# Performance work log

Hardware: AMD Instinct MI355X
Metric: run time of the kernel (lower is better)

Reference implementation:

```python
import jax, jax.numpy as jnp
import numpy as np

B, M, RPI = 16, 80, 256            # images, objects/image, relations/image
N, R = B * M, B * RPI
DF, REP, EMB, HID, NH, L = 12544, 1024, 256, 512, 8, 4
OBJC, RELC = 151, 51
IMW, IMH = 800.0, 600.0


def _ln(x, g, b):
    m = x.mean(-1, keepdims=True)
    v = ((x - m) ** 2).mean(-1, keepdims=True)
    return (x - m) * jax.lax.rsqrt(v + 1e-5) * g + b


def _encoder(x, qkv_w, qkv_b, out_w, out_b, f1_w, f1_b, f2_w, f2_b, ln1_s, ln1_b, ln2_s, ln2_b):
    # post-LN transformer encoder, L layers, x: [B, M, HID]
    Bb, Mm, D = x.shape
    dk = D // NH
    scale = 1.0 / jnp.sqrt(jnp.float32(dk))
    for l in range(L):
        qkv = x @ qkv_w[l].T + qkv_b[l]
        q, k, v = jnp.split(qkv, 3, axis=-1)
        hs = lambda t: t.reshape(Bb, Mm, NH, dk).transpose(0, 2, 1, 3)
        q, k, v = hs(q), hs(k), hs(v)
        att = jax.nn.softmax(jnp.einsum('bhqd,bhkd->bhqk', q, k) * scale, axis=-1)
        o = jnp.einsum('bhqk,bhkd->bhqd', att, v).transpose(0, 2, 1, 3).reshape(Bb, Mm, D)
        x = _ln(x + o @ out_w[l].T + out_b[l], ln1_s[l], ln1_b[l])
        f = jax.nn.relu(x @ f1_w[l].T + f1_b[l]) @ f2_w[l].T + f2_b[l]
        x = _ln(x + f, ln2_s[l], ln2_b[l])
    return x


def _box_info(boxes):
    wh = boxes[:, 2:] - boxes[:, :2] + 1.0
    xy = boxes[:, :2] + 0.5 * wh
    w, h = wh[:, :1], wh[:, 1:]
    x, y = xy[:, :1], xy[:, 1:]
    x1, y1, x2, y2 = boxes[:, 0:1], boxes[:, 1:2], boxes[:, 2:3], boxes[:, 3:4]
    return jnp.concatenate([w / IMW, h / IMH, x / IMW, y / IMH, x1 / IMW, y1 / IMH,
                            x2 / IMW, y2 / IMH, w * h / (IMW * IMH)], axis=-1)  # [N, 9]


def setup_inputs() -> dict:
    key = jax.random.key(0)
    ks = iter(jax.random.split(key, 80))
    nrm = lambda shape, s=0.02: jax.random.normal(next(ks), shape, jnp.float32) * s
    d = {}
    d['features'] = jax.random.normal(next(ks), (N, DF), jnp.float32)
    d['union_features'] = jax.random.normal(next(ks), (R, REP), jnp.float32)
    x1 = jax.random.uniform(next(ks), (N, 1)) * (IMW - 120.0)
    y1 = jax.random.uniform(next(ks), (N, 1)) * (IMH - 120.0)
    w = jax.random.uniform(next(ks), (N, 1)) * 100.0 + 5.0
    h = jax.random.uniform(next(ks), (N, 1)) * 100.0 + 5.0
    d['boxes'] = jnp.concatenate([x1, y1, x1 + w, y1 + h], axis=-1)
    d['logits'] = jax.random.normal(next(ks), (N, OBJC), jnp.float32)
    d['labels'] = jax.random.randint(next(ks), (N,), 0, OBJC)
    d['rel_pair_idxs'] = jax.random.randint(next(ks), (B, RPI, 2), 0, M)
    # feature extractor
    d['fe1_w'] = nrm((REP, DF)); d['fe1_b'] = jnp.zeros((REP,))
    d['fe2_w'] = nrm((REP, REP)); d['fe2_b'] = jnp.zeros((REP,))
    # embeddings
    d['emb1'] = nrm((OBJC, EMB), 1.0)
    d['emb2'] = nrm((OBJC, EMB), 1.0)
    # bbox embed 9->32->128
    d['bb1_w'] = nrm((32, 9)); d['bb1_b'] = jnp.zeros((32,))
    d['bb2_w'] = nrm((128, 32)); d['bb2_b'] = jnp.zeros((128,))
    d['lobj_w'] = nrm((HID, REP + EMB + 128)); d['lobj_b'] = jnp.zeros((HID,))
    d['ledge_w'] = nrm((HID, EMB + HID)); d['ledge_b'] = jnp.zeros((HID,))
    for p in ('o', 'e'):
        d[p + 'qkv_w'] = nrm((L, 3 * HID, HID)); d[p + 'qkv_b'] = jnp.zeros((L, 3 * HID))
        d[p + 'out_w'] = nrm((L, HID, HID)); d[p + 'out_b'] = jnp.zeros((L, HID))
        d[p + 'f1_w'] = nrm((L, HID, HID)); d[p + 'f1_b'] = jnp.zeros((L, HID))
        d[p + 'f2_w'] = nrm((L, HID, HID)); d[p + 'f2_b'] = jnp.zeros((L, HID))
        d[p + 'ln1_s'] = jnp.ones((L, HID)); d[p + 'ln1_b'] = jnp.zeros((L, HID))
        d[p + 'ln2_s'] = jnp.ones((L, HID)); d[p + 'ln2_b'] = jnp.zeros((L, HID))
    d['pcat_w'] = nrm((REP, 2 * HID)); d['pcat_b'] = jnp.zeros((REP,))
    d['fuse_w'] = nrm((REP, REP + HID)); d['fuse_b'] = jnp.zeros((REP,))
    d['cpx_w'] = nrm((RELC, 2 * REP)); d['cpx_b'] = jnp.zeros((RELC,))
    d['dpath_w'] = nrm((RELC, REP)); d['dpath_b'] = jnp.zeros((RELC,))
    return d


def reference(features, union_features, boxes, logits,
              fe1_w, fe1_b, fe2_w, fe2_b, emb1, emb2,
              bb1_w, bb1_b, bb2_w, bb2_b, lobj_w, lobj_b, ledge_w, ledge_b,
              oqkv_w, oqkv_b, oout_w, oout_b, of1_w, of1_b, of2_w, of2_b,
              oln1_s, oln1_b, oln2_s, oln2_b,
              eqkv_w, eqkv_b, eout_w, eout_b, ef1_w, ef1_b, ef2_w, ef2_b,
              eln1_s, eln1_b, eln2_s, eln2_b,
              pcat_w, pcat_b, fuse_w, fuse_b, cpx_w, cpx_b, dpath_w, dpath_b,
              labels, rel_pair_idxs):
    # FeatureExtractor
    bf = jax.nn.relu(features @ fe1_w.T + fe1_b)
    bf = jax.nn.relu(bf @ fe2_w.T + fe2_b)                        # [N, REP]
    # bbox embedding (dropout = identity in eval)
    pos = jax.nn.relu(_box_info(boxes) @ bb1_w.T + bb1_b)
    pos = jax.nn.relu(pos @ bb2_w.T + bb2_b)                      # [N, 128]
    obj_rep = jnp.concatenate([bf, emb1[labels], pos], -1) @ lobj_w.T + lobj_b  # [N, HID]
    obj_emb = _encoder(obj_rep.reshape(B, M, HID), oqkv_w, oqkv_b, oout_w, oout_b,
                       of1_w, of1_b, of2_w, of2_b, oln1_s, oln1_b, oln2_s, oln2_b)  # [B, M, HID]
    edge_in = jnp.concatenate([obj_emb.reshape(N, HID), emb2[labels]], -1) @ ledge_w.T + ledge_b
    gctx = _encoder(edge_in.reshape(B, M, HID), eqkv_w, eqkv_b, eout_w, eout_b,
                    ef1_w, ef1_b, ef2_w, ef2_b, eln1_s, eln1_b, eln2_s, eln2_b).mean(axis=1)  # [B, HID]
    # pair gather per image
    head = jax.vmap(lambda e, i: e[i])(obj_emb, rel_pair_idxs[:, :, 0])  # [B, RPI, HID]
    tail = jax.vmap(lambda e, i: e[i])(obj_emb, rel_pair_idxs[:, :, 1])
    pair = jnp.concatenate([head, tail], -1).reshape(R, 2 * HID)
    local = pair @ pcat_w.T + pcat_b                               # [R, REP]
    gexp = jnp.repeat(gctx, RPI, axis=0)                           # [R, HID]
    sem = jax.nn.relu(jnp.concatenate([local, gexp], -1) @ fuse_w.T + fuse_b)
    final = jnp.concatenate([sem, union_features], -1)             # [R, 2*REP]
    rel_logits = final @ cpx_w.T + cpx_b + local @ dpath_w.T + dpath_b  # [R, RELC]
    return rel_logits
```

## Files before the change

### kernel.cpp

```cpp
#include <hip/hip_runtime.h>
#include <hip/hip_bf16.h>
#include <cstdint>

#define DEV_INLINE __device__ __forceinline__

using u16 = unsigned short;
typedef __attribute__((ext_vector_type(8))) short bf8_t;
typedef __attribute__((ext_vector_type(4))) float f32x4;

constexpr int cB = 16, cM = 80, cRPI = 256;
constexpr int cN = cB * cM;
constexpr int cR = cB * cRPI;
constexpr int cDF = 12544, cREP = 1024, cEMB = 256, cHID = 512, cNH = 8, cL = 4;
constexpr int cRELC = 51;

DEV_INLINE u16 f2bf(float x) { return __builtin_bit_cast(u16, __float2bfloat16(x)); }
DEV_INLINE float bf2f(u16 u) { return __bfloat162float(__builtin_bit_cast(__hip_bfloat16, u)); }

DEV_INLINE float wave_max(float v) {
#pragma unroll
  for (int o = 32; o; o >>= 1) v = fmaxf(v, __shfl_xor(v, o));
  return v;
}
DEV_INLINE float wave_sum(float v) {
#pragma unroll
  for (int o = 32; o; o >>= 1) v += __shfl_xor(v, o);
  return v;
}

DEV_INLINE void gl_lds16(const u16* gp, char* lp) {
  __builtin_amdgcn_global_load_lds(
      (const __attribute__((address_space(1))) void*)gp,
      (__attribute__((address_space(3))) void*)lp, 16, 0, 0);
}

DEV_INLINE void xcd_remap(int& bx, int& by) {
  const int gx = gridDim.x;
  const int nwg = gx * gridDim.y;
  const int id = blockIdx.x + gx * blockIdx.y;
  const int q = nwg >> 3, r = nwg & 7;
  const int x = id & 7, k = id >> 3;
  const int idp = (x < r) ? x * (q + 1) + k : r * (q + 1) + (x - r) * q + k;
  bx = idp % gx;
  by = idp / gx;
}

__global__ __launch_bounds__(256) void gemm_aw(
    const u16* __restrict__ A,
    const u16* __restrict__ W, int ldw,
    float* __restrict__ outF, int ldc,
    u16* __restrict__ outH, int ldh,
    const float* __restrict__ bias,
    const float* __restrict__ res, int resld, int resmode,
    int relu)
{
  __shared__ u16 As[32 * 512];
  const int tid = threadIdx.x;
  const int wid = tid >> 6, lane = tid & 63;
  const int l15 = lane & 15, l4 = lane >> 4;
  int bx, by;
  xcd_remap(bx, by);
  const int bm = by * 32, bn = bx * 32;
  const int wr = wid >> 1, wc = wid & 1;

#pragma unroll
  for (int i = 0; i < 8; ++i) {
    const int c = i * 256 + tid;
    const int row = c >> 6, gran = c & 63;
    const int sg = gran ^ (row & 7);
    gl_lds16(A + (size_t)(bm + row) * 512 + sg * 8,
             (char*)As + (size_t)(i * 256 + wid * 64) * 16);
  }

  const u16* wrow = W + (size_t)(bn + wc * 16 + l15) * ldw + l4 * 8;
  bf8_t wv[16];
#pragma unroll
  for (int ks = 0; ks < 16; ++ks)
    wv[ks] = *(const bf8_t*)&wrow[ks * 32];

  __syncthreads();

  const int ra = wr * 16 + l15;
  f32x4 acc = {};
#pragma unroll
  for (int ks = 0; ks < 16; ++ks) {
    const int ga = ((ks << 2) | l4) ^ (ra & 7);
    const bf8_t af = *(const bf8_t*)&As[ra * 512 + ga * 8];
    acc = __builtin_amdgcn_mfma_f32_16x16x32_bf16(af, wv[ks], acc, 0, 0, 0);
  }

  const int ccol = bn + wc * 16 + l15;
  const float bv = bias ? bias[ccol] : 0.f;
#pragma unroll
  for (int g = 0; g < 4; ++g) {
    const int r = bm + wr * 16 + l4 * 4 + g;
    float v = acc[g] + bv;
    if (resmode == 1) v += res[(size_t)r * resld + ccol];
    if (relu) v = fmaxf(v, 0.f);
    if (outF) outF[(size_t)r * ldc + ccol] = v;
    if (outH) outH[(size_t)r * ldh + ccol] = f2bf(v);
  }
}

static void gaw(hipStream_t s, const u16* A, const u16* W, int ldw, int M, int N,
                float* outF, int ldc, u16* outH, int ldh,
                const float* bias, const float* res, int resld, int resmode, int relu) {
  dim3 g(N / 32, M / 32);
  gemm_aw<<<g, 256, 0, s>>>(A, W, ldw, outF, ldc, outH, ldh, bias, res, resld, resmode, relu);
}

template <int BM, int BN, bool SPLIT>
__global__ __launch_bounds__(256) void gemm_h(
    const u16* __restrict__ A, int lda,
    const u16* __restrict__ Bw, int ldb,
    int Mr, int Nr, int Klen,
    float* __restrict__ outF, int ldc,
    u16* __restrict__ outH, int ldh,
    const float* __restrict__ bias,
    const float* __restrict__ res, int resld, int resmode,
    int relu)
{
  constexpr int MF = BM > 32 ? BM / 32 : 1, NF = BN > 32 ? BN / 32 : 1;
  constexpr int ACH = BM * 4, BCH = BN * 4;
  __shared__ u16 As[2][BM * 32];
  __shared__ u16 Bs[2][BN * 32];
  const int tid = threadIdx.x;
  const int wid = tid >> 6, lane = tid & 63;
  const int l15 = lane & 15, l4 = lane >> 4;
  int bx, by;
  xcd_remap(bx, by);
  const int bm = by * BM, bn = bx * BN;
  const int wr = wid >> 1, wc = wid & 1;
  const int kbase = SPLIT ? blockIdx.z * Klen : 0;

  f32x4 acc[MF][NF] = {};

  auto stage = [&](int buf, int ks) {
    const int k0 = kbase + (ks << 5);
#pragma unroll
    for (int i = 0; i < (ACH + 255) / 256; ++i) {
      const int cA = i * 256 + tid;
      if (ACH % 256 == 0 || cA < ACH) {
        const int row = cA >> 2, seg = cA & 3;
        const int sseg = seg ^ (row & 3);
        gl_lds16(A + (size_t)(bm + row) * lda + k0 + sseg * 8,
                 (char*)As[buf] + (size_t)(cA - lane) * 16);
      }
    }
#pragma unroll
    for (int i = 0; i < (BCH + 255) / 256; ++i) {
      const int cBp = i * 256 + ((tid + 128) & 255);
      if (BCH % 256 == 0 || cBp < BCH) {
        const int row = cBp >> 2, seg = cBp & 3;
        const int sseg = seg ^ (row & 3);
        int brow = bn + row; if (brow > Nr - 1) brow = Nr - 1;
        gl_lds16(Bw + (size_t)brow * ldb + k0 + sseg * 8,
                 (char*)Bs[buf] + (size_t)(cBp - lane) * 16);
      }
    }
  };

  const int nk = Klen >> 5;
  stage(0, 0);
  __syncthreads();

  for (int ks = 0; ks < nk; ++ks) {
    const int cur = ks & 1;
    if (ks + 1 < nk) stage(cur ^ 1, ks + 1);

    bf8_t af[MF], bfr[NF];
#pragma unroll
    for (int m = 0; m < MF; ++m) {
      const int r = wr * (BM / 2) + m * 16 + l15;
      const int g = l4 ^ (r & 3);
      af[m] = *(const bf8_t*)&As[cur][r * 32 + g * 8];
    }
#pragma unroll
    for (int n = 0; n < NF; ++n) {
      const int r = wc * (BN / 2) + n * 16 + l15;
      const int g = l4 ^ (r & 3);
      bfr[n] = *(const bf8_t*)&Bs[cur][r * 32 + g * 8];
    }
#pragma unroll
    for (int m = 0; m < MF; ++m)
#pragma unroll
      for (int n = 0; n < NF; ++n)
        acc[m][n] = __builtin_amdgcn_mfma_f32_16x16x32_bf16(af[m], bfr[n], acc[m][n], 0, 0, 0);
    __syncthreads();
  }

  if (SPLIT) {
    float* po = outF + (size_t)blockIdx.z * Mr * ldc;
#pragma unroll
    for (int m = 0; m < MF; ++m)
#pragma unroll
      for (int n = 0; n < NF; ++n) {
        const int ccol = bn + wc * (BN / 2) + n * 16 + l15;
        if (ccol >= Nr) continue;
#pragma unroll
        for (int g = 0; g < 4; ++g) {
          const int r = bm + wr * (BM / 2) + m * 16 + l4 * 4 + g;
          po[(size_t)r * ldc + ccol] = acc[m][n][g];
        }
      }
  } else {
#pragma unroll
    for (int m = 0; m < MF; ++m)
#pragma unroll
      for (int n = 0; n < NF; ++n) {
        const int ccol = bn + wc * (BN / 2) + n * 16 + l15;
        if (ccol >= Nr) continue;
        const float bv = bias ? bias[ccol] : 0.f;
#pragma unroll
        for (int g = 0; g < 4; ++g) {
          const int r = bm + wr * (BM / 2) + m * 16 + l4 * 4 + g;
          float v = acc[m][n][g] + bv;
          if (resmode == 1) v += res[(size_t)r * resld + ccol];
          else if (resmode == 2) v += res[(size_t)(r >> 8) * resld + ccol];
          if (relu) v = fmaxf(v, 0.f);
          if (outF) outF[(size_t)r * ldc + ccol] = v;
          if (outH) outH[(size_t)r * ldh + ccol] = f2bf(v);
        }
      }
  }
}

template <int BM, int BN>
static void g16(hipStream_t s, const u16* A, int lda, const u16* W, int ldb,
                int M, int N, int K, float* outF, int ldc, u16* outH, int ldh,
                const float* bias, const float* res, int resld, int resmode, int relu) {
  dim3 g((N + BN - 1) / BN, M / BM);
  gemm_h<BM, BN, false><<<g, 256, 0, s>>>(A, lda, W, ldb, M, N, K, outF, ldc, outH, ldh,
                                          bias, res, resld, resmode, relu);
}

__global__ void conv_big2(const float* __restrict__ f, const float* __restrict__ w,
                          u16* __restrict__ fh, u16* __restrict__ wh) {
  constexpr int N1 = cN * cDF / 4;
  constexpr int N2 = cREP * cDF / 4;
  for (int i = blockIdx.x * 256 + threadIdx.x; i < N1 + N2; i += gridDim.x * 256) {
    const float4 v = (i < N1) ? ((const float4*)f)[i] : ((const float4*)w)[i - N1];
    ushort4 o = {f2bf(v.x), f2bf(v.y), f2bf(v.z), f2bf(v.w)};
    if (i < N1) ((ushort4*)fh)[i] = o; else ((ushort4*)wh)[i - N1] = o;
  }
}

constexpr size_t W_FE2 = 0, W_LOBJ = W_FE2 + 1048576, W_LEDGE = W_LOBJ + 720896,
  W_OQKV = W_LEDGE + 393216, W_OOUT = W_OQKV + 3145728, W_OF1 = W_OOUT + 1048576,
  W_OF2 = W_OF1 + 1048576, W_EQKV = W_OF2 + 1048576, W_EOUT = W_EQKV + 3145728,
  W_EF1 = W_EOUT + 1048576, W_EF2 = W_EF1 + 1048576, W_PCAT = W_EF2 + 1048576,
  W_FUSE = W_PCAT + 1048576, W_WEND = W_FUSE + 1572864;

struct EncSrcs {
  const float *fe2, *lobj, *ledge, *oqkv, *oout, *of1, *of2,
              *eqkv, *eout, *ef1, *ef2, *pcat, *fuse;
};

__global__ void conv_enc(EncSrcs S, u16* __restrict__ wb) {
#define SEG(nm, OFF, PRE, LEN) \
  if (i < (PRE) + (LEN)) { \
    const float4 v = ((const float4*)S.nm)[i - (PRE)]; \
    ushort4 o = {f2bf(v.x), f2bf(v.y), f2bf(v.z), f2bf(v.w)}; \
    ((ushort4*)(wb + (OFF)))[i - (PRE)] = o; \
  } else
  for (int i = blockIdx.x * 256 + threadIdx.x; i < (int)(W_WEND / 4); i += gridDim.x * 256) {
    SEG(fe2,  W_FE2,   0,       262144)
    SEG(lobj, W_LOBJ,  262144,  180224)
    SEG(ledge,W_LEDGE, 442368,  98304)
    SEG(oqkv, W_OQKV,  540672,  786432)
    SEG(oout, W_OOUT,  1327104, 262144)
    SEG(of1,  W_OF1,   1589248, 262144)
    SEG(of2,  W_OF2,   1851392, 262144)
    SEG(eqkv, W_EQKV,  2113536, 786432)
    SEG(eout, W_EOUT,  2899968, 262144)
    SEG(ef1,  W_EF1,   3162112, 262144)
    SEG(ef2,  W_EF2,   3424256, 262144)
    SEG(pcat, W_PCAT,  3686400, 262144)
    SEG(fuse, W_FUSE,  3948544, 393216)
    { }
  }
#undef SEG
}

__global__ void conv_cat(const float* __restrict__ cpx, const float* __restrict__ dpath,
                         const float* __restrict__ cb, const float* __restrict__ db,
                         u16* __restrict__ catw, float* __restrict__ biasc) {
  constexpr int N1 = cRELC * 512;
  constexpr int N2 = cRELC * 256;
  const int i0 = blockIdx.x * 256 + threadIdx.x;
  if (blockIdx.x == 0 && threadIdx.x < cRELC) biasc[threadIdx.x] = cb[threadIdx.x] + db[threadIdx.x];
  for (int i = i0; i < N1 + N2; i += gridDim.x * 256) {
    if (i < N1) {
      const int r = i >> 9, c = i & 511;
      const float4 v = ((const float4*)cpx)[i];
      ushort4 o = {f2bf(v.x), f2bf(v.y), f2bf(v.z), f2bf(v.w)};
      ((ushort4*)catw)[r * 768 + c] = o;
    } else {
      const int j = i - N1, r = j >> 8, c = j & 255;
      const float4 v = ((const float4*)dpath)[j];
      ushort4 o = {f2bf(v.x), f2bf(v.y), f2bf(v.z), f2bf(v.w)};
      ((ushort4*)catw)[r * 768 + 512 + c] = o;
    }
  }
}

__global__ void conv2d_kernel(const float* __restrict__ src, int slda,
                              u16* __restrict__ dst, int dld, int cols) {
  const int r = blockIdx.x;
  for (int c = threadIdx.x; c < cols; c += blockDim.x)
    dst[(size_t)r * dld + c] = f2bf(src[(size_t)r * slda + c]);
}

__global__ __launch_bounds__(256) void prep_obj(
    const float* __restrict__ boxes,
    const float* __restrict__ bb1w, const float* __restrict__ bb1b,
    const float* __restrict__ bb2w, const float* __restrict__ bb2b,
    const float* __restrict__ emb1, const int* __restrict__ labels,
    u16* __restrict__ obj_in) {
  __shared__ float W1[288];
  __shared__ float W2[4096];
  __shared__ float P1[8][33];
  const int tid = threadIdx.x;
  for (int i = tid; i < 288; i += 256) W1[i] = bb1w[i];
  for (int i = tid; i < 4096; i += 256) W2[i] = bb2w[i];
  __syncthreads();
  const int r8 = tid >> 5, sub = tid & 31;
  const int row = blockIdx.x * 8 + r8;
  const float x1 = boxes[row * 4], y1 = boxes[row * 4 + 1];
  const float x2 = boxes[row * 4 + 2], y2 = boxes[row * 4 + 3];
  const float w = x2 - x1 + 1.f, h = y2 - y1 + 1.f;
  const float bi[9] = {w / 800.f, h / 600.f, (x1 + 0.5f * w) / 800.f, (y1 + 0.5f * h) / 600.f,
                       x1 / 800.f, y1 / 600.f, x2 / 800.f, y2 / 600.f, w * h / 480000.f};
  float p = bb1b[sub];
#pragma unroll
  for (int j = 0; j < 9; ++j) p += bi[j] * W1[sub * 9 + j];
  P1[r8][sub] = fmaxf(p, 0.f);
  __syncthreads();
#pragma unroll
  for (int jo = 0; jo < 4; ++jo) {
    const int o = sub + jo * 32;
    float a = bb2b[o];
#pragma unroll
    for (int j2 = 0; j2 < 32; ++j2) a += P1[r8][j2] * W2[o * 32 + j2];
    obj_in[(size_t)row * 1408 + 1280 + o] = f2bf(fmaxf(a, 0.f));
  }
  const int l = labels[row];
#pragma unroll
  for (int k = 0; k < 8; ++k)
    obj_in[(size_t)row * 1408 + 1024 + sub + k * 32] = f2bf(emb1[(size_t)l * 256 + sub + k * 32]);
}

__global__ void gather_emb_h(const float* __restrict__ emb, const int* __restrict__ labels,
                             u16* __restrict__ dst, int dld) {
  const int i = blockIdx.x;
  const int l = labels[i];
  const float* s = emb + (size_t)l * cEMB;
  for (int c = threadIdx.x; c < cEMB; c += blockDim.x)
    dst[(size_t)i * dld + c] = f2bf(s[c]);
}

__global__ __launch_bounds__(256) void attn_kernel(const u16* __restrict__ qkv,
                                                   u16* __restrict__ o) {
  __shared__ float Ks[80][65];
  __shared__ float Vs[80][65];
  const int bh = blockIdx.x;
  const int b = bh >> 3, h = bh & 7;
  const int tid = threadIdx.x;
  const u16* base = qkv + (size_t)(b * cM) * 1536 + h * 64;

  for (int e = tid; e < 640; e += 256) {
    const int r = e >> 3, d0 = (e & 7) * 8;
    const bf8_t kv = *(const bf8_t*)&base[(size_t)r * 1536 + 512 + d0];
    const bf8_t vv = *(const bf8_t*)&base[(size_t)r * 1536 + 1024 + d0];
#pragma unroll
    for (int j = 0; j < 8; ++j) {
      Ks[r][d0 + j] = bf2f((u16)kv[j]);
      Vs[r][d0 + j] = bf2f((u16)vv[j]);
    }
  }
  __syncthreads();

  const int wave = tid >> 6, lane = tid & 63;
  const int r0 = blockIdx.y * 16;
  for (int r = r0 + wave; r < r0 + 16; r += 4) {
    const float qd = bf2f(base[(size_t)r * 1536 + lane]);
    const int c2 = 64 + lane;
    const int c2c = (c2 < 80) ? c2 : 0;
    float s0 = 0.f, s1 = 0.f;
#pragma unroll 8
    for (int d = 0; d < 64; ++d) {
      const float qv = __shfl(qd, d);
      s0 += qv * Ks[lane][d];
      s1 += qv * Ks[c2c][d];
    }
    s0 *= 0.125f;
    s1 = (c2 < 80) ? s1 * 0.125f : -1e30f;
    const float mx = wave_max(fmaxf(s0, s1));
    const float p0 = __expf(s0 - mx);
    const float p1 = (c2 < 80) ? __expf(s1 - mx) : 0.f;
    const float ssum = wave_sum(p0 + p1);

    float od = 0.f;
#pragma unroll 8
    for (int c = 0; c < 64; ++c) od += __shfl(p0, c) * Vs[c][lane];
#pragma unroll
    for (int c = 0; c < 16; ++c) od += __shfl(p1, c) * Vs[64 + c][lane];
    od /= ssum;
    o[(size_t)(b * cM + r) * cHID + h * 64 + lane] = f2bf(od);
  }
}

__global__ __launch_bounds__(256) void ln_kernel(
    const float* __restrict__ in, float* __restrict__ outF,
    u16* __restrict__ outH, int ldh,
    const float* __restrict__ g, const float* __restrict__ bta) {
  const int row = blockIdx.x * 4 + (threadIdx.x >> 6);
  const int lane = threadIdx.x & 63;
  const float* x = in + (size_t)row * cHID;
  float v[8];
  float s = 0.f;
#pragma unroll
  for (int i = 0; i < 8; ++i) { v[i] = x[lane + i * 64]; s += v[i]; }
  s = wave_sum(s);
  const float mean = s * (1.f / 512.f);
  float vs = 0.f;
#pragma unroll
  for (int i = 0; i < 8; ++i) { const float d = v[i] - mean; vs += d * d; }
  vs = wave_sum(vs);
  const float inv = rsqrtf(vs * (1.f / 512.f) + 1e-5f);
#pragma unroll
  for (int i = 0; i < 8; ++i) {
    const int c = lane + i * 64;
    const float y = (v[i] - mean) * inv * g[c] + bta[c];
    outF[(size_t)row * cHID + c] = y;
    outH[(size_t)row * ldh + c] = f2bf(y);
  }
}

__global__ void mean_kernel(const float* __restrict__ x, u16* __restrict__ gctx_h) {
  const int b = blockIdx.x;
  const int c = threadIdx.x;
  float s = 0.f;
  for (int m = 0; m < cM; ++m) s += x[(size_t)(b * cM + m) * cHID + c];
  gctx_h[(size_t)b * cHID + c] = f2bf(s * (1.f / 80.f));
}

__global__ void pair_gather_h(const u16* __restrict__ obj, int old, const int* __restrict__ idx,
                              u16* __restrict__ pair) {
  const int r = blockIdx.x;
  const int b = r >> 8, rr = r & 255;
  const int i0 = idx[(size_t)(b * cRPI + rr) * 2 + 0];
  const int i1 = idx[(size_t)(b * cRPI + rr) * 2 + 1];
  const u16* hsrc = obj + (size_t)(b * cM + i0) * old;
  const u16* tsrc = obj + (size_t)(b * cM + i1) * old;
  u16* p = pair + (size_t)r * 1024;
  for (int c = threadIdx.x; c < cHID; c += blockDim.x) {
    p[c] = hsrc[c];
    p[cHID + c] = tsrc[c];
  }
}

__global__ void reduce8_kernel(const float* __restrict__ p, const float* __restrict__ bias,
                               u16* __restrict__ outH) {
  const int idx = blockIdx.x * 256 + threadIdx.x;
  constexpr int total = cN * cREP;
  if (idx >= total) return;
  float v = bias[idx & 1023];
#pragma unroll
  for (int z = 0; z < 8; ++z) v += p[(size_t)z * total + idx];
  outH[idx] = f2bf(fmaxf(v, 0.f));
}

__global__ void freduce_kernel(const float* __restrict__ p, const float* __restrict__ biasc,
                               float* __restrict__ out) {
  const int idx = blockIdx.x * 256 + threadIdx.x;
  if (idx >= cR * cRELC) return;
  const int r = idx / cRELC, c = idx - r * cRELC;
  float v = biasc[c];
#pragma unroll
  for (int z = 0; z < 4; ++z) v += p[(size_t)z * cR * 64 + (size_t)r * 64 + c];
  out[idx] = v;
}

static void run_encoder(hipStream_t s, float* x, u16* xh, u16* qkvh, u16* attn_h,
                        float* res1, u16* f_h,
                        const u16* qkvw, const float* qkvb,
                        const u16* outw, const float* outb,
                        const u16* f1w, const float* f1b,
                        const u16* f2w, const float* f2b,
                        const float* ln1s, const float* ln1b,
                        const float* ln2s, const float* ln2b,
                        u16* last_bf, int last_ld) {
  for (int l = 0; l < cL; ++l) {
    gaw(s, xh, qkvw + (size_t)l * 1536 * 512, 512, cN, 1536,
        nullptr, 0, qkvh, 1536, qkvb + l * 1536, nullptr, 0, 0, 0);
    attn_kernel<<<dim3(cB * cNH, 5), 256, 0, s>>>(qkvh, attn_h);
    gaw(s, attn_h, outw + (size_t)l * 512 * 512, 512, cN, 512,
        res1, 512, nullptr, 0, outb + l * 512, x, 512, 1, 0);
    ln_kernel<<<cN / 4, 256, 0, s>>>(res1, x, xh, 512, ln1s + l * 512, ln1b + l * 512);
    gaw(s, xh, f1w + (size_t)l * 512 * 512, 512, cN, 512,
        nullptr, 0, f_h, 512, f1b + l * 512, nullptr, 0, 0, 1);
    gaw(s, f_h, f2w + (size_t)l * 512 * 512, 512, cN, 512,
        res1, 512, nullptr, 0, f2b + l * 512, x, 512, 1, 0);
    const bool last = (l == cL - 1);
    ln_kernel<<<cN / 4, 256, 0, s>>>(res1, x, last ? last_bf : xh, last ? last_ld : 512,
                                     ln2s + l * 512, ln2b + l * 512);
  }
}

constexpr size_t OFF_FEAT  = 0;
constexpr size_t OFF_FE1W  = 32112640;
constexpr size_t OFF_PART  = 57802752;
constexpr size_t P_END     = 99745792;
constexpr size_t OFF_PAIR  = 0;
constexpr size_t OFF_FINAL = 8388608;
constexpr size_t OFF_OBJIN = 33554432;
constexpr size_t OFF_QKVH  = 37158912;
constexpr size_t OFF_X     = 41091072;
constexpr size_t OFF_XH    = 43712512;
constexpr size_t OFF_ATTN  = 45023232;
constexpr size_t OFF_RES   = 46333952;
constexpr size_t OFF_FH    = 48955392;
constexpr size_t OFF_EDGE  = 50266112;

extern "C" void kernel_launch(void* const* d_in, const int* in_sizes, int n_in,
                              void* d_out, int out_size, void* d_ws, size_t ws_size,
                              hipStream_t stream) {
  (void)in_sizes; (void)n_in; (void)out_size; (void)ws_size;

  const float* features = (const float*)d_in[0];
  const float* unionf   = (const float*)d_in[1];
  const float* boxes    = (const float*)d_in[2];
  const int*   labels   = (const int*)d_in[4];
  const int*   relidx   = (const int*)d_in[5];
  const float* fe1_w = (const float*)d_in[6];
  const float* fe1_b = (const float*)d_in[7];
  const float* fe2_w = (const float*)d_in[8];
  const float* fe2_b = (const float*)d_in[9];
  const float* emb1  = (const float*)d_in[10];
  const float* emb2  = (const float*)d_in[11];
  const float* bb1_w = (const float*)d_in[12];
  const float* bb1_b = (const float*)d_in[13];
  const float* bb2_w = (const float*)d_in[14];
  const float* bb2_b = (const float*)d_in[15];
  const float* lobj_w = (const float*)d_in[16];
  const float* lobj_b = (const float*)d_in[17];
  const float* ledge_w = (const float*)d_in[18];
  const float* ledge_b = (const float*)d_in[19];
  const float* oqkv_w = (const float*)d_in[20];
  const float* oqkv_b = (const float*)d_in[21];
  const float* oout_w = (const float*)d_in[22];
  const float* oout_b = (const float*)d_in[23];
  const float* of1_w = (const float*)d_in[24];
  const float* of1_b = (const float*)d_in[25];
  const float* of2_w = (const float*)d_in[26];
  const float* of2_b = (const float*)d_in[27];
  const float* oln1_s = (const float*)d_in[28];
  const float* oln1_b = (const float*)d_in[29];
  const float* oln2_s = (const float*)d_in[30];
  const float* oln2_b = (const float*)d_in[31];
  const float* eqkv_w = (const float*)d_in[32];
  const float* eqkv_b = (const float*)d_in[33];
  const float* eout_w = (const float*)d_in[34];
  const float* eout_b = (const float*)d_in[35];
  const float* ef1_w = (const float*)d_in[36];
  const float* ef1_b = (const float*)d_in[37];
  const float* ef2_w = (const float*)d_in[38];
  const float* ef2_b = (const float*)d_in[39];
  const float* eln1_s = (const float*)d_in[40];
  const float* eln1_b = (const float*)d_in[41];
  const float* eln2_s = (const float*)d_in[42];
  const float* eln2_b = (const float*)d_in[43];
  const float* pcat_w = (const float*)d_in[44];
  const float* pcat_b = (const float*)d_in[45];
  const float* fuse_w = (const float*)d_in[46];
  const float* fuse_b = (const float*)d_in[47];
  const float* cpx_w  = (const float*)d_in[48];
  const float* cpx_b  = (const float*)d_in[49];
  const float* dpath_w = (const float*)d_in[50];
  const float* dpath_b = (const float*)d_in[51];

  char* wsb = (char*)d_ws;
  u16* feat_h  = (u16*)(wsb + OFF_FEAT);
  u16* fe1w_h  = (u16*)(wsb + OFF_FE1W);
  float* part  = (float*)(wsb + OFF_PART);
  u16* pair    = (u16*)(wsb + OFF_PAIR);
  u16* finalb  = (u16*)(wsb + OFF_FINAL);
  u16* obj_in  = (u16*)(wsb + OFF_OBJIN);
  u16* qkvh    = (u16*)(wsb + OFF_QKVH);
  float* x     = (float*)(wsb + OFF_X);
  u16* xh      = (u16*)(wsb + OFF_XH);
  u16* attn_h  = (u16*)(wsb + OFF_ATTN);
  float* res1  = (float*)(wsb + OFF_RES);
  u16* f_h     = (u16*)(wsb + OFF_FH);
  u16* edge_in = (u16*)(wsb + OFF_EDGE);

  size_t off = P_END;
  auto alloc = [&](size_t bytes) { char* p = wsb + off; off = (off + bytes + 255) & ~(size_t)255; return p; };
  u16* wblock   = (u16*)alloc(W_WEND * 2);
  u16* catw     = (u16*)alloc(313344);
  float* biasc  = (float*)alloc(256);
  u16* bf0h     = (u16*)alloc(2621440);
  u16* gctx_h   = (u16*)alloc(65536);
  float* gcproj = (float*)alloc(262144);
  float* fpart  = (float*)alloc(4194304);

  const u16* fe2w_h   = wblock + W_FE2;
  const u16* lobjw_h  = wblock + W_LOBJ;
  const u16* ledgew_h = wblock + W_LEDGE;
  const u16* pcatw_h  = wblock + W_PCAT;
  const u16* fusew_h  = wblock + W_FUSE;

  conv_big2<<<2048, 256, 0, stream>>>(features, fe1_w, feat_h, fe1w_h);
  EncSrcs es = {fe2_w, lobj_w, ledge_w, oqkv_w, oout_w, of1_w, of2_w,
                eqkv_w, eout_w, ef1_w, ef2_w, pcat_w, fuse_w};
  conv_enc<<<2048, 256, 0, stream>>>(es, wblock);
  conv_cat<<<160, 256, 0, stream>>>(cpx_w, dpath_w, cpx_b, dpath_b, catw, biasc);

  gemm_h<128, 128, true><<<dim3(8, 10, 8), 256, 0, stream>>>(
      feat_h, cDF, fe1w_h, cDF, cN, cREP, cDF / 8, part, cREP,
      nullptr, 0, nullptr, nullptr, 0, 0, 0);
  reduce8_kernel<<<(cN * cREP + 255) / 256, 256, 0, stream>>>(part, fe1_b, bf0h);

  prep_obj<<<cN / 8, 256, 0, stream>>>(boxes, bb1_w, bb1_b, bb2_w, bb2_b, emb1, labels, obj_in);

  g16<32, 32>(stream, bf0h, 1024, fe2w_h, 1024, cN, cREP, cREP,
              nullptr, 0, obj_in, 1408, fe2_b, nullptr, 0, 0, 1);

  g16<32, 32>(stream, obj_in, 1408, lobjw_h, 1408, cN, cHID, 1408,
              x, 512, xh, 512, lobj_b, nullptr, 0, 0, 0);

  run_encoder(stream, x, xh, qkvh, attn_h, res1, f_h,
              wblock + W_OQKV, oqkv_b, wblock + W_OOUT, oout_b,
              wblock + W_OF1, of1_b, wblock + W_OF2, of2_b,
              oln1_s, oln1_b, oln2_s, oln2_b, edge_in, 768);

  gather_emb_h<<<cN, 256, 0, stream>>>(emb2, labels, edge_in + 512, 768);
  pair_gather_h<<<cR, 256, 0, stream>>>(edge_in, 768, relidx, pair);

  g16<32, 32>(stream, edge_in, 768, ledgew_h, 768, cN, cHID, 768,
              x, 512, xh, 512, ledge_b, nullptr, 0, 0, 0);
  run_encoder(stream, x, xh, qkvh, attn_h, res1, f_h,
              wblock + W_EQKV, eqkv_b, wblock + W_EOUT, eout_b,
              wblock + W_EF1, ef1_b, wblock + W_EF2, ef2_b,
              eln1_s, eln1_b, eln2_s, eln2_b, xh, 512);
  mean_kernel<<<cB, cHID, 0, stream>>>(x, gctx_h);

  gaw(stream, gctx_h, fusew_h + 1024, 1536, 64, cREP,
      gcproj, 1024, nullptr, 0, fuse_b, nullptr, 0, 0, 0);

  conv2d_kernel<<<cR, 256, 0, stream>>>(unionf, 1024, finalb + 1024, 3072, 1024);
  g16<128, 64>(stream, pair, 1024, pcatw_h, 1024, cR, cREP, 1024,
               nullptr, 0, finalb + 2048, 3072, pcat_b, nullptr, 0, 0, 0);
  g16<128, 64>(stream, finalb + 2048, 3072, fusew_h, 1536, cR, cREP, 1024,
               nullptr, 0, finalb, 3072, nullptr, gcproj, 1024, 2, 1);

  gemm_h<64, 64, true><<<dim3(1, 64, 4), 256, 0, stream>>>(
      finalb, 3072, catw, 3072, cR, cRELC, 3072 / 4, fpart, 64,
      nullptr, 0, nullptr, nullptr, 0, 0, 0);
  freduce_kernel<<<(cR * cRELC + 255) / 256, 256, 0, stream>>>(fpart, biasc, (float*)d_out);
}
```

Baseline: 973.6 us.

## Specialize fe1 split-K GEMM, drop gemm_aw, fuse embedding and pair gathers

Adds a dedicated gemm_fe1 kernel for the large feature projection. It uses compile-time strides and a 128x128 tile, double-buffered with global-to-LDS loads over 8 K-splits, replacing the generic gemm_h instantiation. The full-K gemm_aw kernel, which staged a 32x512 A tile in LDS and kept all W fragments in registers, is removed. The encoder GEMMs and the gctx projection now go through the tiled g16 path instead. The emb2 label gather and the head/tail pair gather are merged into one launch to save a kernel launch; they touch disjoint columns of edge_in. The specialized kernel's gains depend on the compiler's scheduling, and moving the encoder GEMMs off gemm_aw may cost performance on the small 512-wide layers.

After: 872.0 us, median of 2. -10.4%, faster.

```diff
diff --git a/kernel.cpp b/kernel.cpp
--- a/kernel.cpp
+++ b/kernel.cpp
@@ -45,68 +45,87 @@
   by = idp / gx;
 }
 
-__global__ __launch_bounds__(256) void gemm_aw(
-    const u16* __restrict__ A,
-    const u16* __restrict__ W, int ldw,
-    float* __restrict__ outF, int ldc,
-    u16* __restrict__ outH, int ldh,
-    const float* __restrict__ bias,
-    const float* __restrict__ res, int resld, int resmode,
-    int relu)
+__global__ __launch_bounds__(256) void gemm_fe1(
+    const u16* __restrict__ A, const u16* __restrict__ Bw,
+    float* __restrict__ outF)
 {
-  __shared__ u16 As[32 * 512];
+  constexpr int lda = cDF, ldb = cDF, ldc = cREP;
+  constexpr int Klen = cDF / 8;
+  __shared__ u16 As[2][128 * 32];
+  __shared__ u16 Bs[2][128 * 32];
   const int tid = threadIdx.x;
   const int wid = tid >> 6, lane = tid & 63;
   const int l15 = lane & 15, l4 = lane >> 4;
-  int bx, by;
-  xcd_remap(bx, by);
-  const int bm = by * 32, bn = bx * 32;
+  const int z = blockIdx.x;
+  const int tile = blockIdx.y;
+  const int bm = (tile >> 3) * 128;
+  const int bn = (tile & 7) * 128;
   const int wr = wid >> 1, wc = wid & 1;
-
-#pragma unroll
-  for (int i = 0; i < 8; ++i) {
-    const int c = i * 256 + tid;
-    const int row = c >> 6, gran = c & 63;
-    const int sg = gran ^ (row & 7);
-    gl_lds16(A + (size_t)(bm + row) * 512 + sg * 8,
-             (char*)As + (size_t)(i * 256 + wid * 64) * 16);
-  }
-
-  const u16* wrow = W + (size_t)(bn + wc * 16 + l15) * ldw + l4 * 8;
-  bf8_t wv[16];
-#pragma unroll
-  for (int ks = 0; ks < 16; ++ks)
-    wv[ks] = *(const bf8_t*)&wrow[ks * 32];
-
+  const int kbase = z * Klen;
+
+  f32x4 acc[4][4] = {};
+
+  auto stage = [&](int buf, int ks) {
+    const int k0 = kbase + (ks << 5);
+#pragma unroll
+    for (int i = 0; i < 2; ++i) {
+      const int cA = i * 256 + tid;
+      const int row = cA >> 2, seg = cA & 3;
+      const int sseg = seg ^ (row & 3);
+      gl_lds16(A + (size_t)(bm + row) * lda + k0 + sseg * 8,
+               (char*)As[buf] + (size_t)(cA - lane) * 16);
+    }
+#pragma unroll
+    for (int i = 0; i < 2; ++i) {
+      const int cB2 = i * 256 + tid;
+      const int row = cB2 >> 2, seg = cB2 & 3;
+      const int sseg = seg ^ (row & 3);
+      gl_lds16(Bw + (size_t)(bn + row) * ldb + k0 + sseg * 8,
+               (char*)Bs[buf] + (size_t)(cB2 - lane) * 16);
+    }
+  };
+
+  const int nk = Klen >> 5;
+  stage(0, 0);
   __syncthreads();
 
-  const int ra = wr * 16 + l15;
-  f32x4 acc = {};
-#pragma unroll
-  for (int ks = 0; ks < 16; ++ks) {
-    const int ga = ((ks << 2) | l4) ^ (ra & 7);
-    const bf8_t af = *(const bf8_t*)&As[ra * 512 + ga * 8];
-    acc = __builtin_amdgcn_mfma_f32_16x16x32_bf16(af, wv[ks], acc, 0, 0, 0);
-  }
-
-  const int ccol = bn + wc * 16 + l15;
-  const float bv = bias ? bias[ccol] : 0.f;
-#pragma unroll
-  for (int g = 0; g < 4; ++g) {
-    const int r = bm + wr * 16 + l4 * 4 + g;
-    float v = acc[g] + bv;
-    if (resmode == 1) v += res[(size_t)r * resld + ccol];
-    if (relu) v = fmaxf(v, 0.f);
-    if (outF) outF[(size_t)r * ldc + ccol] = v;
-    if (outH) outH[(size_t)r * ldh + ccol] = f2bf(v);
-  }
-}
-
-static void gaw(hipStream_t s, const u16* A, const u16* W, int ldw, int M, int N,
-                float* outF, int ldc, u16* outH, int ldh,
-                const float* bias, const float* res, int resld, int resmode, int relu) {
-  dim3 g(N / 32, M / 32);
-  gemm_aw<<<g, 256, 0, s>>>(A, W, ldw, outF, ldc, outH, ldh, bias, res, resld, resmode, relu);
+  for (int ks = 0; ks < nk; ++ks) {
+    const int cur = ks & 1;
+    if (ks + 1 < nk) stage(cur ^ 1, ks + 1);
+
+    bf8_t af[4], bfr[4];
+#pragma unroll
+    for (int m = 0; m < 4; ++m) {
+      const int r = wr * 64 + m * 16 + l15;
+      const int g = l4 ^ (r & 3);
+      af[m] = *(const bf8_t*)&As[cur][r * 32 + g * 8];
+    }
+#pragma unroll
+    for (int n = 0; n < 4; ++n) {
+      const int r = wc * 64 + n * 16 + l15;
+      const int g = l4 ^ (r & 3);
+      bfr[n] = *(const bf8_t*)&Bs[cur][r * 32 + g * 8];
+    }
+#pragma unroll
+    for (int m = 0; m < 4; ++m)
+#pragma unroll
+      for (int n = 0; n < 4; ++n)
+        acc[m][n] = __builtin_amdgcn_mfma_f32_16x16x32_bf16(af[m], bfr[n], acc[m][n], 0, 0, 0);
+    __syncthreads();
+  }
+
+  float* po = outF + (size_t)z * cN * ldc;
+#pragma unroll
+  for (int m = 0; m < 4; ++m)
+#pragma unroll
+    for (int n = 0; n < 4; ++n) {
+      const int ccol = bn + wc * 64 + n * 16 + l15;
+#pragma unroll
+      for (int g = 0; g < 4; ++g) {
+        const int r = bm + wr * 64 + m * 16 + l4 * 4 + g;
+        po[(size_t)r * ldc + ccol] = acc[m][n][g];
+      }
+    }
 }
 
 template <int BM, int BN, bool SPLIT>
@@ -350,13 +369,25 @@
     obj_in[(size_t)row * 1408 + 1024 + sub + k * 32] = f2bf(emb1[(size_t)l * 256 + sub + k * 32]);
 }
 
-__global__ void gather_emb_h(const float* __restrict__ emb, const int* __restrict__ labels,
-                             u16* __restrict__ dst, int dld) {
-  const int i = blockIdx.x;
-  const int l = labels[i];
-  const float* s = emb + (size_t)l * cEMB;
-  for (int c = threadIdx.x; c < cEMB; c += blockDim.x)
-    dst[(size_t)i * dld + c] = f2bf(s[c]);
+__global__ void gather_pair(const float* __restrict__ emb2, const int* __restrict__ labels,
+                            u16* __restrict__ edge_in,
+                            const int* __restrict__ idx, u16* __restrict__ pair) {
+  const int r = blockIdx.x;
+  const int tid = threadIdx.x;
+  if (r < cN) {
+    const int l = labels[r];
+    edge_in[(size_t)r * 768 + 512 + tid] = f2bf(emb2[(size_t)l * cEMB + tid]);
+  }
+  const int b = r >> 8, rr = r & 255;
+  const int i0 = idx[(size_t)(b * cRPI + rr) * 2 + 0];
+  const int i1 = idx[(size_t)(b * cRPI + rr) * 2 + 1];
+  const u16* hsrc = edge_in + (size_t)(b * cM + i0) * 768;
+  const u16* tsrc = edge_in + (size_t)(b * cM + i1) * 768;
+  u16* p = pair + (size_t)r * 1024;
+  for (int c = tid; c < cHID; c += blockDim.x) {
+    p[c] = hsrc[c];
+    p[cHID + c] = tsrc[c];
+  }
 }
 
 __global__ __launch_bounds__(256) void attn_kernel(const u16* __restrict__ qkv,
@@ -445,21 +476,6 @@
   gctx_h[(size_t)b * cHID + c] = f2bf(s * (1.f / 80.f));
 }
 
-__global__ void pair_gather_h(const u16* __restrict__ obj, int old, const int* __restrict__ idx,
-                              u16* __restrict__ pair) {
-  const int r = blockIdx.x;
-  const int b = r >> 8, rr = r & 255;
-  const int i0 = idx[(size_t)(b * cRPI + rr) * 2 + 0];
-  const int i1 = idx[(size_t)(b * cRPI + rr) * 2 + 1];
-  const u16* hsrc = obj + (size_t)(b * cM + i0) * old;
-  const u16* tsrc = obj + (size_t)(b * cM + i1) * old;
-  u16* p = pair + (size_t)r * 1024;
-  for (int c = threadIdx.x; c < cHID; c += blockDim.x) {
-    p[c] = hsrc[c];
-    p[cHID + c] = tsrc[c];
-  }
-}
-
 __global__ void reduce8_kernel(const float* __restrict__ p, const float* __restrict__ bias,
                                u16* __restrict__ outH) {
   const int idx = blockIdx.x * 256 + threadIdx.x;
@@ -492,16 +508,16 @@
                         const float* ln2s, const float* ln2b,
                         u16* last_bf, int last_ld) {
   for (int l = 0; l < cL; ++l) {
-    gaw(s, xh, qkvw + (size_t)l * 1536 * 512, 512, cN, 1536,
-        nullptr, 0, qkvh, 1536, qkvb + l * 1536, nullptr, 0, 0, 0);
+    g16<32, 32>(s, xh, 512, qkvw + (size_t)l * 1536 * 512, 512, cN, 1536, 512,
+                nullptr, 0, qkvh, 1536, qkvb + l * 1536, nullptr, 0, 0, 0);
     attn_kernel<<<dim3(cB * cNH, 5), 256, 0, s>>>(qkvh, attn_h);
-    gaw(s, attn_h, outw + (size_t)l * 512 * 512, 512, cN, 512,
-        res1, 512, nullptr, 0, outb + l * 512, x, 512, 1, 0);
+    g16<32, 32>(s, attn_h, 512, outw + (size_t)l * 512 * 512, 512, cN, 512, 512,
+                res1, 512, nullptr, 0, outb + l * 512, x, 512, 1, 0);
     ln_kernel<<<cN / 4, 256, 0, s>>>(res1, x, xh, 512, ln1s + l * 512, ln1b + l * 512);
-    gaw(s, xh, f1w + (size_t)l * 512 * 512, 512, cN, 512,
-        nullptr, 0, f_h, 512, f1b + l * 512, nullptr, 0, 0, 1);
-    gaw(s, f_h, f2w + (size_t)l * 512 * 512, 512, cN, 512,
-        res1, 512, nullptr, 0, f2b + l * 512, x, 512, 1, 0);
+    g16<32, 32>(s, xh, 512, f1w + (size_t)l * 512 * 512, 512, cN, 512, 512,
+                nullptr, 0, f_h, 512, f1b + l * 512, nullptr, 0, 0, 1);
+    g16<32, 32>(s, f_h, 512, f2w + (size_t)l * 512 * 512, 512, cN, 512, 512,
+                res1, 512, nullptr, 0, f2b + l * 512, x, 512, 1, 0);
     const bool last = (l == cL - 1);
     ln_kernel<<<cN / 4, 256, 0, s>>>(res1, x, last ? last_bf : xh, last ? last_ld : 512,
                                      ln2s + l * 512, ln2b + l * 512);
@@ -617,9 +633,7 @@
   conv_enc<<<2048, 256, 0, stream>>>(es, wblock);
   conv_cat<<<160, 256, 0, stream>>>(cpx_w, dpath_w, cpx_b, dpath_b, catw, biasc);
 
-  gemm_h<128, 128, true><<<dim3(8, 10, 8), 256, 0, stream>>>(
-      feat_h, cDF, fe1w_h, cDF, cN, cREP, cDF / 8, part, cREP,
-      nullptr, 0, nullptr, nullptr, 0, 0, 0);
+  gemm_fe1<<<dim3(8, 80), 256, 0, stream>>>(feat_h, fe1w_h, part);
   reduce8_kernel<<<(cN * cREP + 255) / 256, 256, 0, stream>>>(part, fe1_b, bf0h);
 
   prep_obj<<<cN / 8, 256, 0, stream>>>(boxes, bb1_w, bb1_b, bb2_w, bb2_b, emb1, labels, obj_in);
@@ -635,8 +649,7 @@
               wblock + W_OF1, of1_b, wblock + W_OF2, of2_b,
               oln1_s, oln1_b, oln2_s, oln2_b, edge_in, 768);
 
-  gather_emb_h<<<cN, 256, 0, stream>>>(emb2, labels, edge_in + 512, 768);
-  pair_gather_h<<<cR, 256, 0, stream>>>(edge_in, 768, relidx, pair);
+  gather_pair<<<cR, 256, 0, stream>>>(emb2, labels, edge_in, relidx, pair);
 
   g16<32, 32>(stream, edge_in, 768, ledgew_h, 768, cN, cHID, 768,
               x, 512, xh, 512, ledge_b, nullptr, 0, 0, 0);
@@ -646,8 +659,8 @@
               eln1_s, eln1_b, eln2_s, eln2_b, xh, 512);
   mean_kernel<<<cB, cHID, 0, stream>>>(x, gctx_h);
 
-  gaw(stream, gctx_h, fusew_h + 1024, 1536, 64, cREP,
-      gcproj, 1024, nullptr, 0, fuse_b, nullptr, 0, 0, 0);
+  g16<32, 64>(stream, gctx_h, 512, fusew_h + 1024, 1536, 64, cREP, 512,
+              gcproj, 1024, nullptr, 0, fuse_b, nullptr, 0, 0, 0);
 
   conv2d_kernel<<<cR, 256, 0, stream>>>(unionf, 1024, finalb + 1024, 3072, 1024);
   g16<128, 64>(stream, pair, 1024, pcatw_h, 1024, cR, cREP, 1024,
```
